# Kernel tuning notes

Hardware: AMD Instinct MI355X
Metric: run time of the kernel (lower is better)

The kernel has to match this reference:

```python
import jax, jax.numpy as jnp
import numpy as np

B, N_CGS, N_ATOMS, KNN, K, DEPTH = 16, 256, 1024, 32, 128, 3
CUTOFF = 10.0


def _init_params(key):
    ks = jax.random.split(key, 12)
    s = 1.0 / np.sqrt(K)
    p = {}
    # stacked per-depth settransform weights: Linear stored as [in, out] (y = x @ W + b)
    p['mlp_W1'] = jax.random.normal(ks[0], (DEPTH, K, K), jnp.float32) * s
    p['mlp_b1'] = jnp.zeros((DEPTH, K), jnp.float32)
    p['mlp_W2'] = jax.random.normal(ks[1], (DEPTH, K, K), jnp.float32) * s
    p['mlp_b2'] = jnp.zeros((DEPTH, K), jnp.float32)
    p['upd_W1'] = jax.random.normal(ks[2], (DEPTH, K, K), jnp.float32) * s
    p['upd_b1'] = jnp.zeros((DEPTH, K), jnp.float32)
    p['upd_W2'] = jax.random.normal(ks[3], (DEPTH, K, K), jnp.float32) * s
    p['upd_b2'] = jnp.zeros((DEPTH, K), jnp.float32)
    p['dec_W1'] = jax.random.normal(ks[4], (K, K), jnp.float32) * s
    p['dec_b1'] = jnp.zeros((K,), jnp.float32)
    p['dec_W2'] = jax.random.normal(ks[5], (K, N_ATOMS), jnp.float32) * s
    p['dec_b2'] = jnp.zeros((N_ATOMS,), jnp.float32)
    return p


def setup_inputs() -> dict:
    key = jax.random.key(0)
    ks = jax.random.split(key, 6)
    inp = {
        'soft_assign': jax.random.uniform(ks[0], (B, N_ATOMS, N_CGS), jnp.float32),
        'xyz': jax.random.normal(ks[1], (B, N_ATOMS, 3), jnp.float32),
        'cg_xyz': jax.random.normal(ks[2], (B, N_CGS, 3), jnp.float32),
        'assign_norm': jax.random.uniform(ks[3], (B, N_ATOMS, N_CGS), jnp.float32),
        'assign_idx': jax.random.randint(ks[4], (N_ATOMS,), 0, N_CGS, jnp.int32),
    }
    inp.update(_init_params(ks[5]))
    return inp


def _forward(cg_xyz, assign_norm, assign_idx,
             mlp_W1, mlp_b1, mlp_W2, mlp_b2,
             upd_W1, upd_b1, upd_W2, upd_b2,
             dec_W1, dec_b1, dec_W2, dec_b2):
    act = jax.nn.relu
    # Pairwise CG distance + ascending sort (as in source). The source then
    # zeroes sorted values beyond rank knn and uses value.nonzero()[:, 1:] as
    # neighbor pairs, i.e. it indexes by SORT RANK (ranks 1..knn), not by the
    # sorted index tensor knbrs. For generic (distinct) coordinates this is
    # exactly: neighbor j in {1..knn} for every center i. We replicate that.
    dist_vec = cg_xyz[:, None, 1:KNN + 1, :] - cg_xyz[:, :, None, :]  # [B, n_cgs, knn, 3]
    dist_vec = dist_vec.reshape(B, N_CGS * KNN, 3)
    dist = jnp.sqrt(jnp.sum(dist_vec ** 2, axis=-1)).reshape(B, N_CGS, KNN, 1)

    # GaussianSmearing(0, cutoff, feature_dim)
    offset = jnp.linspace(0.0, CUTOFF, K)  # [K]
    coeff = -0.5 / (offset[1] - offset[0]) ** 2
    out = jnp.exp(coeff * (dist - offset) ** 2)  # [B, n_cgs, knn, K]

    # settransform layers (loop over small fixed depth)
    for d in range(DEPTH):
        upd = act(out @ mlp_W1[d] + mlp_b1[d]) @ mlp_W2[d] + mlp_b2[d]
        cg_contract = jnp.mean(upd, axis=-2, keepdims=True)  # mean over knn axis
        h = upd + cg_contract
        out = act(h @ upd_W1[d] + upd_b1[d]) @ upd_W2[d] + upd_b2[d]

    # decode K -> n_atoms
    coeffs = (act(out @ dec_W1 + dec_b1) @ dec_W2 + dec_b2)
    coeffs = coeffs.reshape(B, N_CGS * KNN, N_ATOMS)

    dx_recon = jnp.einsum('bio,bin->bon', coeffs, dist_vec)      # [B, n_atoms, 3]
    cg_offset = jnp.einsum('bin,bij->bjn', dx_recon, assign_norm)  # [B, n_cgs, 3]
    cg_offset_lift = cg_offset[:, assign_idx, :]                  # [B, n_atoms, 3]
    xyz_recon = cg_xyz[:, assign_idx, :] - cg_offset_lift + dx_recon
    return xyz_recon


def reference(soft_assign, xyz, cg_xyz, assign_norm, assign_idx,
              mlp_W1, mlp_b1, mlp_W2, mlp_b2,
              upd_W1, upd_b1, upd_W2, upd_b2,
              dec_W1, dec_b1, dec_W2, dec_b2):
    xyz_recon = _forward(cg_xyz, assign_norm, assign_idx,
                         mlp_W1, mlp_b1, mlp_W2, mlp_b2,
                         upd_W1, upd_b1, upd_W2, upd_b2,
                         dec_W1, dec_b1, dec_W2, dec_b2)
    return (soft_assign, xyz, xyz_recon)
```

## Files before the change

kernel.cpp:

```cpp
#include <hip/hip_runtime.h>

#define BATCH   16
#define NCGS    256
#define NATOMS  1024
#define KNN     32
#define KF      128
#define NSLICE  8

typedef __attribute__((ext_vector_type(8))) short bf16x8;
typedef __attribute__((ext_vector_type(4))) float f32x4;

#define NFRAG (13*8*4)

union U16B { bf16x8 v; uint u[4]; };

__global__ __launch_bounds__(256)
void prep_kernel(const float* __restrict__ mlp_W1, const float* __restrict__ mlp_W2,
                 const float* __restrict__ upd_W1, const float* __restrict__ upd_W2,
                 const float* __restrict__ dec_W1, uint* __restrict__ Wswz)
{
    int t = blockIdx.x * 256 + threadIdx.x;
    if (t >= 13*8*4*64) return;
    int lane = t & 63;
    int kc   = (t >> 6) & 3;
    int ft   = (t >> 8) & 7;
    int s    = t >> 11;

    const float* W;
    if (s < 12) {
        int d = s >> 2, ph = s & 3;
        if      (ph == 0) W = mlp_W1 + d*KF*KF;
        else if (ph == 1) W = mlp_W2 + d*KF*KF;
        else if (ph == 2) W = upd_W1 + d*KF*KF;
        else              W = upd_W2 + d*KF*KF;
    } else W = dec_W1;

    int f = ft*16 + (lane & 15);
    int g = lane >> 4;

    uint hi[4], lo[4];
    #pragma unroll
    for (int w = 0; w < 4; ++w) {
        int k0;
        if (s == 0) k0 = kc*32 + g*8 + 2*w;
        else        k0 = kc*16 + (w>>1)*64 + g*4 + 2*(w&1);
        float v0 = W[(size_t)k0*KF + f];
        float v1 = W[(size_t)(k0+1)*KF + f];
        uint b0 = __float_as_uint(v0), b1 = __float_as_uint(v1);
        hi[w] = (b0 >> 16) | (b1 & 0xffff0000u);
        float l0 = v0 - __uint_as_float(b0 & 0xffff0000u);
        float l1 = v1 - __uint_as_float(b1 & 0xffff0000u);
        lo[w] = (__float_as_uint(l0) >> 16) | (__float_as_uint(l1) & 0xffff0000u);
    }
    int fi = (s*8 + ft)*4 + kc;
    uint* ph_ = Wswz + (size_t)((fi*2 + 0)*64 + lane)*4;
    uint* pl_ = Wswz + (size_t)((fi*2 + 1)*64 + lane)*4;
    #pragma unroll
    for (int w = 0; w < 4; ++w) { ph_[w] = hi[w]; pl_[w] = lo[w]; }
}

__device__ __forceinline__ void gload_lds16(const void* g, void* l)
{
    __builtin_amdgcn_global_load_lds(
        (const __attribute__((address_space(1))) void*)g,
        (__attribute__((address_space(3))) void*)l, 16, 0, 0);
}

__device__ __forceinline__ void stage_half(const char* __restrict__ Wbase,
                                           int s, int hf, char* buf, int wv, int l)
{
    #pragma unroll
    for (int q = 0; q < 8; ++q) {
        int j   = wv*8 + q;
        int kc2 = j >> 4, ft = (j >> 1) & 7, p = j & 1;
        int fi  = (s*8 + ft)*4 + (2*hf + kc2);
        const char* g = Wbase + ((size_t)(fi*2 + p))*1024 + (size_t)l*16;
        gload_lds16(g, buf + (size_t)j*1024);
    }
}

template<int KC, int FH>
__device__ __forceinline__ void comp_grp(const char* buf, int l,
        const bf16x8 (&bh)[2][4], const bf16x8 (&bl)[2][4], f32x4 (&acc)[8][2])
{
    constexpr int KC2 = KC & 1;
    #pragma unroll
    for (int i = 0; i < 4; ++i) {
        const int ft = FH*4 + i;
        bf16x8 whi = *(const bf16x8*)(buf + (size_t)(((KC2*8 + ft)*2 + 0)*1024) + (size_t)l*16);
        bf16x8 wlo = *(const bf16x8*)(buf + (size_t)(((KC2*8 + ft)*2 + 1)*1024) + (size_t)l*16);
        #pragma unroll
        for (int rt = 0; rt < 2; ++rt) {
            acc[ft][rt] = __builtin_amdgcn_mfma_f32_16x16x32_bf16(whi, bh[rt][KC], acc[ft][rt], 0, 0, 0);
            acc[ft][rt] = __builtin_amdgcn_mfma_f32_16x16x32_bf16(whi, bl[rt][KC], acc[ft][rt], 0, 0, 0);
            acc[ft][rt] = __builtin_amdgcn_mfma_f32_16x16x32_bf16(wlo, bh[rt][KC], acc[ft][rt], 0, 0, 0);
        }
    }
}

__global__ __launch_bounds__(256, 2)
void mlp_kernel(const float* __restrict__ cg_xyz, const char* __restrict__ Wf,
                const float* __restrict__ mlp_b1, const float* __restrict__ mlp_b2,
                const float* __restrict__ upd_b1, const float* __restrict__ upd_b2,
                const float* __restrict__ dec_b1, float* __restrict__ Gp)
{
    __shared__ __align__(16) char Wlds[2][32*1024];

    const int tid = threadIdx.x;
    const int wv  = tid >> 6;
    const int l   = tid & 63;
    const int g   = l >> 4;
    const int e0  = l & 15;
    const int b   = blockIdx.x >> 6;
    const int cg  = (blockIdx.x & 63) * 4 + wv;

    stage_half(Wf, 0, 0, Wlds[0], wv, l);

    const float* cgb = cg_xyz + (size_t)b * NCGS * 3;
    const float cx = cgb[cg*3+0], cy = cgb[cg*3+1], cz = cgb[cg*3+2];
    const float d0x = cgb[(1+e0)*3+0]-cx,  d0y = cgb[(1+e0)*3+1]-cy,  d0z = cgb[(1+e0)*3+2]-cz;
    const float d1x = cgb[(17+e0)*3+0]-cx, d1y = cgb[(17+e0)*3+1]-cy, d1z = cgb[(17+e0)*3+2]-cz;
    const float dist0 = sqrtf(d0x*d0x + d0y*d0y + d0z*d0z);
    const float dist1 = sqrtf(d1x*d1x + d1y*d1y + d1z*d1z);

    const float STEP  = 10.0f / 127.0f;
    const float COEFF = -0.5f / (STEP * STEP);
    bf16x8 bh[2][4], bl[2][4];
    #pragma unroll
    for (int rt = 0; rt < 2; ++rt) {
        float dd = rt ? dist1 : dist0;
        #pragma unroll
        for (int kc = 0; kc < 4; ++kc) {
            U16B H, L;
            #pragma unroll
            for (int w = 0; w < 4; ++w) {
                int k0 = kc*32 + g*8 + 2*w;
                float t0 = dd - (float)k0 * STEP;
                float t1 = dd - (float)(k0+1) * STEP;
                float e0f = __expf(COEFF * t0 * t0);
                float e1f = __expf(COEFF * t1 * t1);
                uint b0 = __float_as_uint(e0f), b1 = __float_as_uint(e1f);
                H.u[w] = (b0 >> 16) | (b1 & 0xffff0000u);
                float l0 = e0f - __uint_as_float(b0 & 0xffff0000u);
                float l1 = e1f - __uint_as_float(b1 & 0xffff0000u);
                L.u[w] = (__float_as_uint(l0) >> 16) | (__float_as_uint(l1) & 0xffff0000u);
            }
            bh[rt][kc] = H.v; bl[rt][kc] = L.v;
        }
    }

    asm volatile("s_waitcnt vmcnt(0)" ::: "memory");
    __syncthreads();

    f32x4 acc[8][2];
    for (int s = 0; s < 13; ++s) {
        const float* bias; int md;
        {
            int d = s >> 2, ph = s & 3;
            if      (s == 12)  { bias = dec_b1;        md = 0; }
            else if (ph == 0)  { bias = mlp_b1 + d*KF; md = 0; }
            else if (ph == 1)  { bias = mlp_b2 + d*KF; md = 1; }
            else if (ph == 2)  { bias = upd_b1 + d*KF; md = 0; }
            else               { bias = upd_b2 + d*KF; md = 2; }
        }

        stage_half(Wf, s, 1, Wlds[1], wv, l);

        #pragma unroll
        for (int ft = 0; ft < 8; ++ft) {
            float4 bv = *(const float4*)(bias + ft*16 + g*4);
            acc[ft][0] = (f32x4){bv.x, bv.y, bv.z, bv.w};
            acc[ft][1] = acc[ft][0];
        }

        comp_grp<0,0>(Wlds[0], l, bh, bl, acc);
        comp_grp<0,1>(Wlds[0], l, bh, bl, acc);
        comp_grp<1,0>(Wlds[0], l, bh, bl, acc);
        comp_grp<1,1>(Wlds[0], l, bh, bl, acc);

        asm volatile("s_waitcnt vmcnt(0)" ::: "memory");
        __syncthreads();

        if (s < 12) stage_half(Wf, s+1, 0, Wlds[0], wv, l);

        comp_grp<2,0>(Wlds[1], l, bh, bl, acc);
        comp_grp<2,1>(Wlds[1], l, bh, bl, acc);
        comp_grp<3,0>(Wlds[1], l, bh, bl, acc);
        comp_grp<3,1>(Wlds[1], l, bh, bl, acc);

        if (md == 0) {
            #pragma unroll
            for (int ft = 0; ft < 8; ++ft)
                #pragma unroll
                for (int rt = 0; rt < 2; ++rt)
                    #pragma unroll
                    for (int q = 0; q < 4; ++q)
                        acc[ft][rt][q] = fmaxf(acc[ft][rt][q], 0.f);
        } else if (md == 1) {
            #pragma unroll
            for (int ft = 0; ft < 8; ++ft)
                #pragma unroll
                for (int q = 0; q < 4; ++q) {
                    float sm = acc[ft][0][q] + acc[ft][1][q];
                    sm += __shfl_xor(sm, 1);
                    sm += __shfl_xor(sm, 2);
                    sm += __shfl_xor(sm, 4);
                    sm += __shfl_xor(sm, 8);
                    float mn = sm * (1.0f / 32.0f);
                    acc[ft][0][q] += mn;
                    acc[ft][1][q] += mn;
                }
        }

        if (s < 12) {
            #pragma unroll
            for (int rt = 0; rt < 2; ++rt)
                #pragma unroll
                for (int kc = 0; kc < 4; ++kc) {
                    float v0 = acc[kc  ][rt][0], v1 = acc[kc  ][rt][1];
                    float v2 = acc[kc  ][rt][2], v3 = acc[kc  ][rt][3];
                    float v4 = acc[kc+4][rt][0], v5 = acc[kc+4][rt][1];
                    float v6 = acc[kc+4][rt][2], v7 = acc[kc+4][rt][3];
                    uint u0=__float_as_uint(v0), u1=__float_as_uint(v1);
                    uint u2=__float_as_uint(v2), u3=__float_as_uint(v3);
                    uint u4=__float_as_uint(v4), u5=__float_as_uint(v5);
                    uint u6=__float_as_uint(v6), u7=__float_as_uint(v7);
                    U16B H, L;
                    H.u[0] = (u0>>16)|(u1&0xffff0000u);
                    H.u[1] = (u2>>16)|(u3&0xffff0000u);
                    H.u[2] = (u4>>16)|(u5&0xffff0000u);
                    H.u[3] = (u6>>16)|(u7&0xffff0000u);
                    float l0=v0-__uint_as_float(u0&0xffff0000u), l1=v1-__uint_as_float(u1&0xffff0000u);
                    float l2=v2-__uint_as_float(u2&0xffff0000u), l3=v3-__uint_as_float(u3&0xffff0000u);
                    float l4=v4-__uint_as_float(u4&0xffff0000u), l5=v5-__uint_as_float(u5&0xffff0000u);
                    float l6=v6-__uint_as_float(u6&0xffff0000u), l7=v7-__uint_as_float(u7&0xffff0000u);
                    L.u[0] = (__float_as_uint(l0)>>16)|(__float_as_uint(l1)&0xffff0000u);
                    L.u[1] = (__float_as_uint(l2)>>16)|(__float_as_uint(l3)&0xffff0000u);
                    L.u[2] = (__float_as_uint(l4)>>16)|(__float_as_uint(l5)&0xffff0000u);
                    L.u[3] = (__float_as_uint(l6)>>16)|(__float_as_uint(l7)&0xffff0000u);
                    bh[rt][kc] = H.v; bl[rt][kc] = L.v;
                }
        }

        asm volatile("s_waitcnt vmcnt(0)" ::: "memory");
        __syncthreads();
    }

    const int slice = blockIdx.x & (NSLICE-1);
    float* Gb = Gp + ((size_t)slice*BATCH + b) * KF * 3;
    #pragma unroll
    for (int ft = 0; ft < 8; ++ft) {
        #pragma unroll
        for (int q = 0; q < 4; ++q) {
            float r0 = acc[ft][0][q], r1 = acc[ft][1][q];
            float px = r0*d0x + r1*d1x;
            float py = r0*d0y + r1*d1y;
            float pz = r0*d0z + r1*d1z;
            px += __shfl_xor(px, 1); py += __shfl_xor(py, 1); pz += __shfl_xor(pz, 1);
            px += __shfl_xor(px, 2); py += __shfl_xor(py, 2); pz += __shfl_xor(pz, 2);
            px += __shfl_xor(px, 4); py += __shfl_xor(py, 4); pz += __shfl_xor(pz, 4);
            px += __shfl_xor(px, 8); py += __shfl_xor(py, 8); pz += __shfl_xor(pz, 8);
            if (e0 < 3) {
                float pv = (e0 == 0) ? px : ((e0 == 1) ? py : pz);
                atomicAdd(Gb + (16*ft + 4*g + q)*3 + e0, pv);
            }
        }
    }
}

__global__ __launch_bounds__(256)
void dx_kernel(const float* __restrict__ cg_xyz, const float* __restrict__ dec_W2,
               const float* __restrict__ dec_b2, const float* __restrict__ Gp,
               float* __restrict__ dxr)
{
    __shared__ float Gl[KF * 3];
    __shared__ float red[256 * 3];
    const int tid = threadIdx.x;
    const int b   = blockIdx.x >> 2;
    const int og  = blockIdx.x & 3;

    if (tid < 192) {
        float s0 = 0.f, s1 = 0.f;
        #pragma unroll
        for (int sl = 0; sl < NSLICE; ++sl) {
            const float* gp = Gp + ((size_t)sl*BATCH + b) * KF * 3;
            s0 += gp[tid]; s1 += gp[tid + 192];
        }
        Gl[tid] = s0; Gl[tid + 192] = s1;
    }
    const float* cgb = cg_xyz + (size_t)b * NCGS * 3;
    float w = ((tid >= 1 && tid <= 32) ? 256.f : 0.f) - 32.f;
    red[tid]       = w * cgb[tid*3+0];
    red[256 + tid] = w * cgb[tid*3+1];
    red[512 + tid] = w * cgb[tid*3+2];
    __syncthreads();
    for (int s2 = 128; s2 > 0; s2 >>= 1) {
        if (tid < s2) {
            red[tid]       += red[tid + s2];
            red[256 + tid] += red[256 + tid + s2];
            red[512 + tid] += red[512 + tid + s2];
        }
        __syncthreads();
    }
    const float S0 = red[0], S1 = red[256], S2 = red[512];

    const int o = og * 256 + tid;
    const float bq = dec_b2[o];
    float a0 = bq * S0, a1 = bq * S1, a2 = bq * S2;
    #pragma unroll 4
    for (int k = 0; k < KF; ++k) {
        float wvv = dec_W2[k * NATOMS + o];
        a0 = fmaf(wvv, Gl[k*3+0], a0);
        a1 = fmaf(wvv, Gl[k*3+1], a1);
        a2 = fmaf(wvv, Gl[k*3+2], a2);
    }
    float* dp = dxr + ((size_t)b * NATOMS + o) * 3;
    dp[0] = a0; dp[1] = a1; dp[2] = a2;
}

__global__ __launch_bounds__(256)
void cgo_kernel(const float* __restrict__ assign_norm, const float* __restrict__ dxr,
                float* __restrict__ cgo)
{
    __shared__ float dxl[64 * 3];
    const int tid = threadIdx.x;
    const int b   = blockIdx.x >> 4;
    const int a0  = (blockIdx.x & 15) * 64;
    if (tid < 192) dxl[tid] = dxr[((size_t)b * NATOMS + a0) * 3 + tid];
    __syncthreads();
    float c0 = 0.f, c1 = 0.f, c2 = 0.f;
    const float* an = assign_norm + ((size_t)b * NATOMS + a0) * NCGS + tid;
    #pragma unroll 4
    for (int a = 0; a < 64; ++a) {
        float v = an[(size_t)a * NCGS];
        c0 = fmaf(v, dxl[a*3+0], c0);
        c1 = fmaf(v, dxl[a*3+1], c1);
        c2 = fmaf(v, dxl[a*3+2], c2);
    }
    float* cp = cgo + ((size_t)b * NCGS + tid) * 3;
    atomicAdd(cp+0, c0); atomicAdd(cp+1, c1); atomicAdd(cp+2, c2);
}

__global__ __launch_bounds__(256)
void recon_kernel(const float* __restrict__ cg_xyz, const float* __restrict__ cgo,
                  const float* __restrict__ dxr, const int* __restrict__ assign_idx,
                  float* __restrict__ out)
{
    int i = blockIdx.x * 256 + threadIdx.x;
    int b   = i / (NATOMS * 3);
    int rem = i - b * (NATOMS * 3);
    int a   = rem / 3;
    int n   = rem - a * 3;
    int ia  = assign_idx[a];
    float v = cg_xyz[((size_t)b*NCGS + ia)*3 + n]
            - cgo[((size_t)b*NCGS + ia)*3 + n]
            + dxr[((size_t)b*NATOMS + a)*3 + n];
    out[i] = v;
}

extern "C" void kernel_launch(void* const* d_in, const int* in_sizes, int n_in,
                              void* d_out, int out_size, void* d_ws, size_t ws_size,
                              hipStream_t stream)
{
    const float* soft_assign = (const float*)d_in[0];
    const float* xyz         = (const float*)d_in[1];
    const float* cg_xyz      = (const float*)d_in[2];
    const float* assign_norm = (const float*)d_in[3];
    const int*   assign_idx  = (const int*)  d_in[4];
    const float* mlp_W1 = (const float*)d_in[5];
    const float* mlp_b1 = (const float*)d_in[6];
    const float* mlp_W2 = (const float*)d_in[7];
    const float* mlp_b2 = (const float*)d_in[8];
    const float* upd_W1 = (const float*)d_in[9];
    const float* upd_b1 = (const float*)d_in[10];
    const float* upd_W2 = (const float*)d_in[11];
    const float* upd_b2 = (const float*)d_in[12];
    const float* dec_W1 = (const float*)d_in[13];
    const float* dec_b1 = (const float*)d_in[14];
    const float* dec_W2 = (const float*)d_in[15];
    const float* dec_b2 = (const float*)d_in[16];

    float* out = (float*)d_out;

    uint*  Wswz = (uint*)d_ws;
    float* Gp   = (float*)d_ws + NFRAG*2*64*4;
    float* cgo  = Gp + NSLICE * BATCH * KF * 3;
    float* dxr  = cgo + BATCH * NCGS * 3;

    hipMemcpyAsync(out, soft_assign, (size_t)BATCH*NATOMS*NCGS*sizeof(float),
                   hipMemcpyDeviceToDevice, stream);
    hipMemcpyAsync(out + (size_t)BATCH*NATOMS*NCGS, xyz,
                   (size_t)BATCH*NATOMS*3*sizeof(float),
                   hipMemcpyDeviceToDevice, stream);
    hipMemsetAsync(Gp, 0,
        (size_t)(NSLICE*BATCH*KF*3 + BATCH*NCGS*3)*sizeof(float), stream);

    prep_kernel<<<104, 256, 0, stream>>>(mlp_W1, mlp_W2, upd_W1, upd_W2, dec_W1, Wswz);
    mlp_kernel<<<BATCH*64, 256, 0, stream>>>(cg_xyz, (const char*)Wswz,
        mlp_b1, mlp_b2, upd_b1, upd_b2, dec_b1, Gp);
    dx_kernel<<<BATCH*4, 256, 0, stream>>>(cg_xyz, dec_W2, dec_b2, Gp, dxr);
    cgo_kernel<<<BATCH*16, 256, 0, stream>>>(assign_norm, dxr, cgo);
    recon_kernel<<<(BATCH*NATOMS*3)/256, 256, 0, stream>>>(
        cg_xyz, cgo, dxr, assign_idx,
        out + (size_t)BATCH*NATOMS*NCGS + (size_t)BATCH*NATOMS*3);
}
```

Baseline: 301.2 us.

## Process two CG centers per wave to reuse staged weight fragments

Each wave now handles two coarse-grain centers (four row tiles) instead of one, so each weight fragment read from LDS feeds twice as many MFMAs. The grid is halved to 512 blocks and launch bounds drop to one block per CU so the larger accumulator and operand arrays fit in registers. The aim is to cut global-to-LDS weight staging and LDS reads per unit of work. The cost is lower occupancy, less latency hiding, and fewer blocks to spread across CUs.

```diff
diff --git a/kernel.cpp b/kernel.cpp
--- a/kernel.cpp
+++ b/kernel.cpp
@@ -81,7 +81,7 @@
 
 template<int KC, int FH>
 __device__ __forceinline__ void comp_grp(const char* buf, int l,
-        const bf16x8 (&bh)[2][4], const bf16x8 (&bl)[2][4], f32x4 (&acc)[8][2])
+        const bf16x8 (&bh)[4][4], const bf16x8 (&bl)[4][4], f32x4 (&acc)[8][4])
 {
     constexpr int KC2 = KC & 1;
     #pragma unroll
@@ -90,7 +90,7 @@
         bf16x8 whi = *(const bf16x8*)(buf + (size_t)(((KC2*8 + ft)*2 + 0)*1024) + (size_t)l*16);
         bf16x8 wlo = *(const bf16x8*)(buf + (size_t)(((KC2*8 + ft)*2 + 1)*1024) + (size_t)l*16);
         #pragma unroll
-        for (int rt = 0; rt < 2; ++rt) {
+        for (int rt = 0; rt < 4; ++rt) {
             acc[ft][rt] = __builtin_amdgcn_mfma_f32_16x16x32_bf16(whi, bh[rt][KC], acc[ft][rt], 0, 0, 0);
             acc[ft][rt] = __builtin_amdgcn_mfma_f32_16x16x32_bf16(whi, bl[rt][KC], acc[ft][rt], 0, 0, 0);
             acc[ft][rt] = __builtin_amdgcn_mfma_f32_16x16x32_bf16(wlo, bh[rt][KC], acc[ft][rt], 0, 0, 0);
@@ -98,7 +98,7 @@
     }
 }
 
-__global__ __launch_bounds__(256, 2)
+__global__ __launch_bounds__(256, 1)
 void mlp_kernel(const float* __restrict__ cg_xyz, const char* __restrict__ Wf,
                 const float* __restrict__ mlp_b1, const float* __restrict__ mlp_b2,
                 const float* __restrict__ upd_b1, const float* __restrict__ upd_b2,
@@ -111,24 +111,33 @@
     const int l   = tid & 63;
     const int g   = l >> 4;
     const int e0  = l & 15;
-    const int b   = blockIdx.x >> 6;
-    const int cg  = (blockIdx.x & 63) * 4 + wv;
+    const int b   = blockIdx.x >> 5;
+    const int cg0 = (blockIdx.x & 31) * 8 + wv * 2;
 
     stage_half(Wf, 0, 0, Wlds[0], wv, l);
 
     const float* cgb = cg_xyz + (size_t)b * NCGS * 3;
-    const float cx = cgb[cg*3+0], cy = cgb[cg*3+1], cz = cgb[cg*3+2];
-    const float d0x = cgb[(1+e0)*3+0]-cx,  d0y = cgb[(1+e0)*3+1]-cy,  d0z = cgb[(1+e0)*3+2]-cz;
-    const float d1x = cgb[(17+e0)*3+0]-cx, d1y = cgb[(17+e0)*3+1]-cy, d1z = cgb[(17+e0)*3+2]-cz;
-    const float dist0 = sqrtf(d0x*d0x + d0y*d0y + d0z*d0z);
-    const float dist1 = sqrtf(d1x*d1x + d1y*d1y + d1z*d1z);
+    float ex[4], ey[4], ez[4], ds[4];
+    #pragma unroll
+    for (int c = 0; c < 2; ++c) {
+        const int cgc = cg0 + c;
+        const float cx = cgb[cgc*3+0], cy = cgb[cgc*3+1], cz = cgb[cgc*3+2];
+        #pragma unroll
+        for (int rth = 0; rth < 2; ++rth) {
+            const int nb = 1 + rth*16 + e0;
+            const int t  = c*2 + rth;
+            float dx = cgb[nb*3+0]-cx, dy = cgb[nb*3+1]-cy, dz = cgb[nb*3+2]-cz;
+            ex[t] = dx; ey[t] = dy; ez[t] = dz;
+            ds[t] = sqrtf(dx*dx + dy*dy + dz*dz);
+        }
+    }
 
     const float STEP  = 10.0f / 127.0f;
     const float COEFF = -0.5f / (STEP * STEP);
-    bf16x8 bh[2][4], bl[2][4];
-    #pragma unroll
-    for (int rt = 0; rt < 2; ++rt) {
-        float dd = rt ? dist1 : dist0;
+    bf16x8 bh[4][4], bl[4][4];
+    #pragma unroll
+    for (int rt = 0; rt < 4; ++rt) {
+        float dd = ds[rt];
         #pragma unroll
         for (int kc = 0; kc < 4; ++kc) {
             U16B H, L;
@@ -152,7 +161,7 @@
     asm volatile("s_waitcnt vmcnt(0)" ::: "memory");
     __syncthreads();
 
-    f32x4 acc[8][2];
+    f32x4 acc[8][4];
     for (int s = 0; s < 13; ++s) {
         const float* bias; int md;
         {
@@ -171,6 +180,8 @@
             float4 bv = *(const float4*)(bias + ft*16 + g*4);
             acc[ft][0] = (f32x4){bv.x, bv.y, bv.z, bv.w};
             acc[ft][1] = acc[ft][0];
+            acc[ft][2] = acc[ft][0];
+            acc[ft][3] = acc[ft][0];
         }
 
         comp_grp<0,0>(Wlds[0], l, bh, bl, acc);
@@ -192,7 +203,7 @@
             #pragma unroll
             for (int ft = 0; ft < 8; ++ft)
                 #pragma unroll
-                for (int rt = 0; rt < 2; ++rt)
+                for (int rt = 0; rt < 4; ++rt)
                     #pragma unroll
                     for (int q = 0; q < 4; ++q)
                         acc[ft][rt][q] = fmaxf(acc[ft][rt][q], 0.f);
@@ -201,20 +212,22 @@
             for (int ft = 0; ft < 8; ++ft)
                 #pragma unroll
                 for (int q = 0; q < 4; ++q) {
-                    float sm = acc[ft][0][q] + acc[ft][1][q];
-                    sm += __shfl_xor(sm, 1);
-                    sm += __shfl_xor(sm, 2);
-                    sm += __shfl_xor(sm, 4);
-                    sm += __shfl_xor(sm, 8);
-                    float mn = sm * (1.0f / 32.0f);
-                    acc[ft][0][q] += mn;
-                    acc[ft][1][q] += mn;
+                    float sa = acc[ft][0][q] + acc[ft][1][q];
+                    float sb = acc[ft][2][q] + acc[ft][3][q];
+                    sa += __shfl_xor(sa, 1);  sb += __shfl_xor(sb, 1);
+                    sa += __shfl_xor(sa, 2);  sb += __shfl_xor(sb, 2);
+                    sa += __shfl_xor(sa, 4);  sb += __shfl_xor(sb, 4);
+                    sa += __shfl_xor(sa, 8);  sb += __shfl_xor(sb, 8);
+                    float ma = sa * (1.0f / 32.0f);
+                    float mb = sb * (1.0f / 32.0f);
+                    acc[ft][0][q] += ma;  acc[ft][1][q] += ma;
+                    acc[ft][2][q] += mb;  acc[ft][3][q] += mb;
                 }
         }
 
         if (s < 12) {
             #pragma unroll
-            for (int rt = 0; rt < 2; ++rt)
+            for (int rt = 0; rt < 4; ++rt)
                 #pragma unroll
                 for (int kc = 0; kc < 4; ++kc) {
                     float v0 = acc[kc  ][rt][0], v1 = acc[kc  ][rt][1];
@@ -252,10 +265,14 @@
     for (int ft = 0; ft < 8; ++ft) {
         #pragma unroll
         for (int q = 0; q < 4; ++q) {
-            float r0 = acc[ft][0][q], r1 = acc[ft][1][q];
-            float px = r0*d0x + r1*d1x;
-            float py = r0*d0y + r1*d1y;
-            float pz = r0*d0z + r1*d1z;
+            float px = 0.f, py = 0.f, pz = 0.f;
+            #pragma unroll
+            for (int rt = 0; rt < 4; ++rt) {
+                float r = acc[ft][rt][q];
+                px = fmaf(r, ex[rt], px);
+                py = fmaf(r, ey[rt], py);
+                pz = fmaf(r, ez[rt], pz);
+            }
             px += __shfl_xor(px, 1); py += __shfl_xor(py, 1); pz += __shfl_xor(pz, 1);
             px += __shfl_xor(px, 2); py += __shfl_xor(py, 2); pz += __shfl_xor(pz, 2);
             px += __shfl_xor(px, 4); py += __shfl_xor(py, 4); pz += __shfl_xor(pz, 4);
@@ -396,7 +413,7 @@
         (size_t)(NSLICE*BATCH*KF*3 + BATCH*NCGS*3)*sizeof(float), stream);
 
     prep_kernel<<<104, 256, 0, stream>>>(mlp_W1, mlp_W2, upd_W1, upd_W2, dec_W1, Wswz);
-    mlp_kernel<<<BATCH*64, 256, 0, stream>>>(cg_xyz, (const char*)Wswz,
+    mlp_kernel<<<BATCH*32, 256, 0, stream>>>(cg_xyz, (const char*)Wswz,
         mlp_b1, mlp_b2, upd_b1, upd_b2, dec_b1, Gp);
     dx_kernel<<<BATCH*4, 256, 0, stream>>>(cg_xyz, dec_W2, dec_b2, Gp, dxr);
     cgo_kernel<<<BATCH*16, 256, 0, stream>>>(assign_norm, dxr, cgo);
```

New measurement: 334.6 us. 11.1% more time.

## Split each CG's neighbor rows across two waves with quarter-K weight staging

Applied to the files above, without the earlier changes.

The MLP kernel now runs 512 threads per block. Each wave handles one 16-row half of a CG's 32 neighbors, where before one wave held both halves. Per-wave register state (accumulators and bf16 hi/lo operand fragments) is halved, and weight staging moves to four quarter-K LDS buffers with a barrier after each quarter. The knn mean now needs a cross-wave exchange through shared memory plus an extra barrier. The aim is higher occupancy and latency hiding, at the cost of more synchronization and twice as many waves reading the same weight fragments from LDS.

```diff
diff --git a/kernel.cpp b/kernel.cpp
--- a/kernel.cpp
+++ b/kernel.cpp
@@ -66,45 +66,41 @@
         (__attribute__((address_space(3))) void*)l, 16, 0, 0);
 }
 
-__device__ __forceinline__ void stage_half(const char* __restrict__ Wbase,
-                                           int s, int hf, char* buf, int wv, int l)
-{
-    #pragma unroll
-    for (int q = 0; q < 8; ++q) {
-        int j   = wv*8 + q;
-        int kc2 = j >> 4, ft = (j >> 1) & 7, p = j & 1;
-        int fi  = (s*8 + ft)*4 + (2*hf + kc2);
-        const char* g = Wbase + ((size_t)(fi*2 + p))*1024 + (size_t)l*16;
-        gload_lds16(g, buf + (size_t)j*1024);
-    }
-}
-
-template<int KC, int FH>
-__device__ __forceinline__ void comp_grp(const char* buf, int l,
-        const bf16x8 (&bh)[2][4], const bf16x8 (&bl)[2][4], f32x4 (&acc)[8][2])
-{
-    constexpr int KC2 = KC & 1;
-    #pragma unroll
-    for (int i = 0; i < 4; ++i) {
-        const int ft = FH*4 + i;
-        bf16x8 whi = *(const bf16x8*)(buf + (size_t)(((KC2*8 + ft)*2 + 0)*1024) + (size_t)l*16);
-        bf16x8 wlo = *(const bf16x8*)(buf + (size_t)(((KC2*8 + ft)*2 + 1)*1024) + (size_t)l*16);
-        #pragma unroll
-        for (int rt = 0; rt < 2; ++rt) {
-            acc[ft][rt] = __builtin_amdgcn_mfma_f32_16x16x32_bf16(whi, bh[rt][KC], acc[ft][rt], 0, 0, 0);
-            acc[ft][rt] = __builtin_amdgcn_mfma_f32_16x16x32_bf16(whi, bl[rt][KC], acc[ft][rt], 0, 0, 0);
-            acc[ft][rt] = __builtin_amdgcn_mfma_f32_16x16x32_bf16(wlo, bh[rt][KC], acc[ft][rt], 0, 0, 0);
-        }
-    }
-}
-
-__global__ __launch_bounds__(256, 2)
+__device__ __forceinline__ void stage_quarter(const char* __restrict__ Wbase,
+                                              int s, int kc, char* buf, int wv, int l)
+{
+    #pragma unroll
+    for (int q = 0; q < 2; ++q) {
+        int j  = wv*2 + q;
+        int ft = j >> 1, p = j & 1;
+        int fi = (s*8 + ft)*4 + kc;
+        const char* gp = Wbase + ((size_t)(fi*2 + p))*1024 + (size_t)l*16;
+        gload_lds16(gp, buf + (size_t)j*1024);
+    }
+}
+
+template<int KC>
+__device__ __forceinline__ void comp_q(const char* buf, int l,
+        const bf16x8 (&bh)[4], const bf16x8 (&bl)[4], f32x4 (&acc)[8])
+{
+    #pragma unroll
+    for (int ft = 0; ft < 8; ++ft) {
+        bf16x8 whi = *(const bf16x8*)(buf + (size_t)((ft*2+0)*1024) + (size_t)l*16);
+        bf16x8 wlo = *(const bf16x8*)(buf + (size_t)((ft*2+1)*1024) + (size_t)l*16);
+        acc[ft] = __builtin_amdgcn_mfma_f32_16x16x32_bf16(whi, bh[KC], acc[ft], 0, 0, 0);
+        acc[ft] = __builtin_amdgcn_mfma_f32_16x16x32_bf16(whi, bl[KC], acc[ft], 0, 0, 0);
+        acc[ft] = __builtin_amdgcn_mfma_f32_16x16x32_bf16(wlo, bh[KC], acc[ft], 0, 0, 0);
+    }
+}
+
+__global__ __launch_bounds__(512, 4)
 void mlp_kernel(const float* __restrict__ cg_xyz, const char* __restrict__ Wf,
                 const float* __restrict__ mlp_b1, const float* __restrict__ mlp_b2,
                 const float* __restrict__ upd_b1, const float* __restrict__ upd_b2,
                 const float* __restrict__ dec_b1, float* __restrict__ Gp)
 {
-    __shared__ __align__(16) char Wlds[2][32*1024];
+    __shared__ __align__(16) char Wlds[2][16*1024];
+    __shared__ float meanb[8*KF];
 
     const int tid = threadIdx.x;
     const int wv  = tid >> 6;
@@ -112,47 +108,43 @@
     const int g   = l >> 4;
     const int e0  = l & 15;
     const int b   = blockIdx.x >> 6;
-    const int cg  = (blockIdx.x & 63) * 4 + wv;
-
-    stage_half(Wf, 0, 0, Wlds[0], wv, l);
+    const int cg  = (blockIdx.x & 63)*4 + (wv >> 1);
+    const int rth = wv & 1;
+
+    stage_quarter(Wf, 0, 0, Wlds[0], wv, l);
 
     const float* cgb = cg_xyz + (size_t)b * NCGS * 3;
     const float cx = cgb[cg*3+0], cy = cgb[cg*3+1], cz = cgb[cg*3+2];
-    const float d0x = cgb[(1+e0)*3+0]-cx,  d0y = cgb[(1+e0)*3+1]-cy,  d0z = cgb[(1+e0)*3+2]-cz;
-    const float d1x = cgb[(17+e0)*3+0]-cx, d1y = cgb[(17+e0)*3+1]-cy, d1z = cgb[(17+e0)*3+2]-cz;
-    const float dist0 = sqrtf(d0x*d0x + d0y*d0y + d0z*d0z);
-    const float dist1 = sqrtf(d1x*d1x + d1y*d1y + d1z*d1z);
+    const int nb = 1 + rth*16 + e0;
+    const float ex = cgb[nb*3+0]-cx, ey = cgb[nb*3+1]-cy, ez = cgb[nb*3+2]-cz;
+    const float dist = sqrtf(ex*ex + ey*ey + ez*ez);
 
     const float STEP  = 10.0f / 127.0f;
     const float COEFF = -0.5f / (STEP * STEP);
-    bf16x8 bh[2][4], bl[2][4];
-    #pragma unroll
-    for (int rt = 0; rt < 2; ++rt) {
-        float dd = rt ? dist1 : dist0;
+    bf16x8 bh[4], bl[4];
+    #pragma unroll
+    for (int kc = 0; kc < 4; ++kc) {
+        U16B H, L;
         #pragma unroll
-        for (int kc = 0; kc < 4; ++kc) {
-            U16B H, L;
-            #pragma unroll
-            for (int w = 0; w < 4; ++w) {
-                int k0 = kc*32 + g*8 + 2*w;
-                float t0 = dd - (float)k0 * STEP;
-                float t1 = dd - (float)(k0+1) * STEP;
-                float e0f = __expf(COEFF * t0 * t0);
-                float e1f = __expf(COEFF * t1 * t1);
-                uint b0 = __float_as_uint(e0f), b1 = __float_as_uint(e1f);
-                H.u[w] = (b0 >> 16) | (b1 & 0xffff0000u);
-                float l0 = e0f - __uint_as_float(b0 & 0xffff0000u);
-                float l1 = e1f - __uint_as_float(b1 & 0xffff0000u);
-                L.u[w] = (__float_as_uint(l0) >> 16) | (__float_as_uint(l1) & 0xffff0000u);
-            }
-            bh[rt][kc] = H.v; bl[rt][kc] = L.v;
-        }
+        for (int w = 0; w < 4; ++w) {
+            int k0 = kc*32 + g*8 + 2*w;
+            float t0 = dist - (float)k0 * STEP;
+            float t1 = dist - (float)(k0+1) * STEP;
+            float e0f = __expf(COEFF * t0 * t0);
+            float e1f = __expf(COEFF * t1 * t1);
+            uint b0 = __float_as_uint(e0f), b1 = __float_as_uint(e1f);
+            H.u[w] = (b0 >> 16) | (b1 & 0xffff0000u);
+            float l0 = e0f - __uint_as_float(b0 & 0xffff0000u);
+            float l1 = e1f - __uint_as_float(b1 & 0xffff0000u);
+            L.u[w] = (__float_as_uint(l0) >> 16) | (__float_as_uint(l1) & 0xffff0000u);
+        }
+        bh[kc] = H.v; bl[kc] = L.v;
     }
 
     asm volatile("s_waitcnt vmcnt(0)" ::: "memory");
     __syncthreads();
 
-    f32x4 acc[8][2];
+    f32x4 acc[8];
     for (int s = 0; s < 13; ++s) {
         const float* bias; int md;
         {
@@ -164,86 +156,92 @@
             else               { bias = upd_b2 + d*KF; md = 2; }
         }
 
-        stage_half(Wf, s, 1, Wlds[1], wv, l);
+        stage_quarter(Wf, s, 1, Wlds[1], wv, l);
 
         #pragma unroll
         for (int ft = 0; ft < 8; ++ft) {
             float4 bv = *(const float4*)(bias + ft*16 + g*4);
-            acc[ft][0] = (f32x4){bv.x, bv.y, bv.z, bv.w};
-            acc[ft][1] = acc[ft][0];
-        }
-
-        comp_grp<0,0>(Wlds[0], l, bh, bl, acc);
-        comp_grp<0,1>(Wlds[0], l, bh, bl, acc);
-        comp_grp<1,0>(Wlds[0], l, bh, bl, acc);
-        comp_grp<1,1>(Wlds[0], l, bh, bl, acc);
-
+            acc[ft] = (f32x4){bv.x, bv.y, bv.z, bv.w};
+        }
+
+        comp_q<0>(Wlds[0], l, bh, bl, acc);
         asm volatile("s_waitcnt vmcnt(0)" ::: "memory");
         __syncthreads();
 
-        if (s < 12) stage_half(Wf, s+1, 0, Wlds[0], wv, l);
-
-        comp_grp<2,0>(Wlds[1], l, bh, bl, acc);
-        comp_grp<2,1>(Wlds[1], l, bh, bl, acc);
-        comp_grp<3,0>(Wlds[1], l, bh, bl, acc);
-        comp_grp<3,1>(Wlds[1], l, bh, bl, acc);
+        stage_quarter(Wf, s, 2, Wlds[0], wv, l);
+        comp_q<1>(Wlds[1], l, bh, bl, acc);
+        asm volatile("s_waitcnt vmcnt(0)" ::: "memory");
+        __syncthreads();
+
+        stage_quarter(Wf, s, 3, Wlds[1], wv, l);
+        comp_q<2>(Wlds[0], l, bh, bl, acc);
+        asm volatile("s_waitcnt vmcnt(0)" ::: "memory");
+        __syncthreads();
+
+        if (s < 12) stage_quarter(Wf, s+1, 0, Wlds[0], wv, l);
+        comp_q<3>(Wlds[1], l, bh, bl, acc);
+        asm volatile("s_waitcnt vmcnt(0)" ::: "memory");
+        __syncthreads();
 
         if (md == 0) {
             #pragma unroll
             for (int ft = 0; ft < 8; ++ft)
                 #pragma unroll
-                for (int rt = 0; rt < 2; ++rt)
-                    #pragma unroll
-                    for (int q = 0; q < 4; ++q)
-                        acc[ft][rt][q] = fmaxf(acc[ft][rt][q], 0.f);
+                for (int q = 0; q < 4; ++q)
+                    acc[ft][q] = fmaxf(acc[ft][q], 0.f);
         } else if (md == 1) {
+            f32x4 own[8];
             #pragma unroll
-            for (int ft = 0; ft < 8; ++ft)
+            for (int ft = 0; ft < 8; ++ft) {
+                f32x4 sm = acc[ft];
                 #pragma unroll
                 for (int q = 0; q < 4; ++q) {
-                    float sm = acc[ft][0][q] + acc[ft][1][q];
-                    sm += __shfl_xor(sm, 1);
-                    sm += __shfl_xor(sm, 2);
-                    sm += __shfl_xor(sm, 4);
-                    sm += __shfl_xor(sm, 8);
-                    float mn = sm * (1.0f / 32.0f);
-                    acc[ft][0][q] += mn;
-                    acc[ft][1][q] += mn;
+                    sm[q] += __shfl_xor(sm[q], 1);
+                    sm[q] += __shfl_xor(sm[q], 2);
+                    sm[q] += __shfl_xor(sm[q], 4);
+                    sm[q] += __shfl_xor(sm[q], 8);
                 }
+                own[ft] = sm;
+                if (e0 == 0)
+                    *(f32x4*)&meanb[wv*KF + ft*16 + g*4] = sm;
+            }
+            __syncthreads();
+            #pragma unroll
+            for (int ft = 0; ft < 8; ++ft) {
+                f32x4 pr = *(const f32x4*)&meanb[(wv^1)*KF + ft*16 + g*4];
+                #pragma unroll
+                for (int q = 0; q < 4; ++q)
+                    acc[ft][q] += (own[ft][q] + pr[q]) * (1.0f / 32.0f);
+            }
         }
 
         if (s < 12) {
             #pragma unroll
-            for (int rt = 0; rt < 2; ++rt)
-                #pragma unroll
-                for (int kc = 0; kc < 4; ++kc) {
-                    float v0 = acc[kc  ][rt][0], v1 = acc[kc  ][rt][1];
-                    float v2 = acc[kc  ][rt][2], v3 = acc[kc  ][rt][3];
-                    float v4 = acc[kc+4][rt][0], v5 = acc[kc+4][rt][1];
-                    float v6 = acc[kc+4][rt][2], v7 = acc[kc+4][rt][3];
-                    uint u0=__float_as_uint(v0), u1=__float_as_uint(v1);
-                    uint u2=__float_as_uint(v2), u3=__float_as_uint(v3);
-                    uint u4=__float_as_uint(v4), u5=__float_as_uint(v5);
-                    uint u6=__float_as_uint(v6), u7=__float_as_uint(v7);
-                    U16B H, L;
-                    H.u[0] = (u0>>16)|(u1&0xffff0000u);
-                    H.u[1] = (u2>>16)|(u3&0xffff0000u);
-                    H.u[2] = (u4>>16)|(u5&0xffff0000u);
-                    H.u[3] = (u6>>16)|(u7&0xffff0000u);
-                    float l0=v0-__uint_as_float(u0&0xffff0000u), l1=v1-__uint_as_float(u1&0xffff0000u);
-                    float l2=v2-__uint_as_float(u2&0xffff0000u), l3=v3-__uint_as_float(u3&0xffff0000u);
-                    float l4=v4-__uint_as_float(u4&0xffff0000u), l5=v5-__uint_as_float(u5&0xffff0000u);
-                    float l6=v6-__uint_as_float(u6&0xffff0000u), l7=v7-__uint_as_float(u7&0xffff0000u);
-                    L.u[0] = (__float_as_uint(l0)>>16)|(__float_as_uint(l1)&0xffff0000u);
-                    L.u[1] = (__float_as_uint(l2)>>16)|(__float_as_uint(l3)&0xffff0000u);
-                    L.u[2] = (__float_as_uint(l4)>>16)|(__float_as_uint(l5)&0xffff0000u);
-                    L.u[3] = (__float_as_uint(l6)>>16)|(__float_as_uint(l7)&0xffff0000u);
-                    bh[rt][kc] = H.v; bl[rt][kc] = L.v;
-                }
-        }
-
-        asm volatile("s_waitcnt vmcnt(0)" ::: "memory");
-        __syncthreads();
+            for (int kc = 0; kc < 4; ++kc) {
+                float v0 = acc[kc  ][0], v1 = acc[kc  ][1];
+                float v2 = acc[kc  ][2], v3 = acc[kc  ][3];
+                float v4 = acc[kc+4][0], v5 = acc[kc+4][1];
+                float v6 = acc[kc+4][2], v7 = acc[kc+4][3];
+                uint u0=__float_as_uint(v0), u1=__float_as_uint(v1);
+                uint u2=__float_as_uint(v2), u3=__float_as_uint(v3);
+                uint u4=__float_as_uint(v4), u5=__float_as_uint(v5);
+                uint u6=__float_as_uint(v6), u7=__float_as_uint(v7);
+                U16B H, L;
+                H.u[0] = (u0>>16)|(u1&0xffff0000u);
+                H.u[1] = (u2>>16)|(u3&0xffff0000u);
+                H.u[2] = (u4>>16)|(u5&0xffff0000u);
+                H.u[3] = (u6>>16)|(u7&0xffff0000u);
+                float l0=v0-__uint_as_float(u0&0xffff0000u), l1=v1-__uint_as_float(u1&0xffff0000u);
+                float l2=v2-__uint_as_float(u2&0xffff0000u), l3=v3-__uint_as_float(u3&0xffff0000u);
+                float l4=v4-__uint_as_float(u4&0xffff0000u), l5=v5-__uint_as_float(u5&0xffff0000u);
+                float l6=v6-__uint_as_float(u6&0xffff0000u), l7=v7-__uint_as_float(u7&0xffff0000u);
+                L.u[0] = (__float_as_uint(l0)>>16)|(__float_as_uint(l1)&0xffff0000u);
+                L.u[1] = (__float_as_uint(l2)>>16)|(__float_as_uint(l3)&0xffff0000u);
+                L.u[2] = (__float_as_uint(l4)>>16)|(__float_as_uint(l5)&0xffff0000u);
+                L.u[3] = (__float_as_uint(l6)>>16)|(__float_as_uint(l7)&0xffff0000u);
+                bh[kc] = H.v; bl[kc] = L.v;
+            }
+        }
     }
 
     const int slice = blockIdx.x & (NSLICE-1);
@@ -252,10 +250,8 @@
     for (int ft = 0; ft < 8; ++ft) {
         #pragma unroll
         for (int q = 0; q < 4; ++q) {
-            float r0 = acc[ft][0][q], r1 = acc[ft][1][q];
-            float px = r0*d0x + r1*d1x;
-            float py = r0*d0y + r1*d1y;
-            float pz = r0*d0z + r1*d1z;
+            float r = acc[ft][q];
+            float px = r*ex, py = r*ey, pz = r*ez;
             px += __shfl_xor(px, 1); py += __shfl_xor(py, 1); pz += __shfl_xor(pz, 1);
             px += __shfl_xor(px, 2); py += __shfl_xor(py, 2); pz += __shfl_xor(pz, 2);
             px += __shfl_xor(px, 4); py += __shfl_xor(py, 4); pz += __shfl_xor(pz, 4);
@@ -396,7 +392,7 @@
         (size_t)(NSLICE*BATCH*KF*3 + BATCH*NCGS*3)*sizeof(float), stream);
 
     prep_kernel<<<104, 256, 0, stream>>>(mlp_W1, mlp_W2, upd_W1, upd_W2, dec_W1, Wswz);
-    mlp_kernel<<<BATCH*64, 256, 0, stream>>>(cg_xyz, (const char*)Wswz,
+    mlp_kernel<<<BATCH*64, 512, 0, stream>>>(cg_xyz, (const char*)Wswz,
         mlp_b1, mlp_b2, upd_b1, upd_b2, dec_b1, Gp);
     dx_kernel<<<BATCH*4, 256, 0, stream>>>(cg_xyz, dec_W2, dec_b2, Gp, dxr);
     cgo_kernel<<<BATCH*16, 256, 0, stream>>>(assign_norm, dxr, cgo);
```

New measurement: 393.5 us. 30.6% more time.
